# Optimization experiments

Hardware: AMD Instinct MI355X
Metric: run time of the kernel (lower is better)

## Reference

```python
import jax, jax.numpy as jnp
import numpy as np

D = 256   # input_dim (also per-head dim)
H = 8     # num_heads
B = 32
S = 1024


def setup_inputs() -> dict:
    key = jax.random.key(0)
    ks = jax.random.split(key, 9)
    scale = 1.0 / np.sqrt(D)
    x = jax.random.normal(ks[0], (B, S, D), dtype=jnp.float32)
    Wk = jax.random.normal(ks[1], (D, D * H), dtype=jnp.float32) * scale
    bk = jnp.zeros((D * H,), dtype=jnp.float32)
    Wv = jax.random.normal(ks[2], (D, D * H), dtype=jnp.float32) * scale
    bv = jnp.zeros((D * H,), dtype=jnp.float32)
    query = jax.random.normal(ks[3], (H, D), dtype=jnp.float32)
    Wo = jax.random.normal(ks[4], (D * H, D), dtype=jnp.float32) / np.sqrt(D * H)
    bo = jnp.zeros((D,), dtype=jnp.float32)
    return {"x": x, "Wk": Wk, "bk": bk, "Wv": Wv, "bv": bv,
            "query": query, "Wo": Wo, "bo": bo}


def reference(x, Wk, bk, Wv, bv, query, Wo, bo):
    b, s, _ = x.shape
    # keys/values: [B, S, H, D]
    keys = (x @ Wk + bk).reshape(b, s, H, D)
    values = (x @ Wv + bv).reshape(b, s, H, D)
    # per-head single-query scores over sequence: [B, S, H]
    scores = jnp.einsum("bshd,hd->bsh", keys, query)
    attn = jax.nn.softmax(scores, axis=1)
    # attention-pooled values per head: [B, H, D] -> concat [B, H*D]
    pooled = jnp.einsum("bsh,bshd->bhd", attn, values).reshape(b, H * D)
    return pooled @ Wo + bo
```

## Files before the change

### kernel.cpp

```cpp
#include <hip/hip_runtime.h>

#define D 256
#define H 8
#define B 32
#define S 1024
#define SCH 32
#define SCS 32
#define XPAD 4

#define OFF_QK   0
#define OFF_ML   2048
#define OFF_XWP  18432

__global__ void __launch_bounds__(256) k_prep(
        const float* __restrict__ Wk, const float* __restrict__ query,
        const float* __restrict__ bo, float* __restrict__ qk,
        float* __restrict__ out) {
    const int h  = blockIdx.x >> 5;
    const int kc = blockIdx.x & 31;
    const int t  = threadIdx.x;
    const int kl = t >> 5;
    const int dq = t & 31;
    const int k  = kc * 8 + kl;
    const int d0 = dq * 8;
    const float* wrow = Wk + (size_t)k * (D * H) + h * D + d0;
    const float* qrow = query + h * D + d0;
    const float4 w0 = *(const float4*)(wrow);
    const float4 w1 = *(const float4*)(wrow + 4);
    const float4 q0 = *(const float4*)(qrow);
    const float4 q1 = *(const float4*)(qrow + 4);
    float acc = w0.x * q0.x + w0.y * q0.y + w0.z * q0.z + w0.w * q0.w
              + w1.x * q1.x + w1.y * q1.y + w1.z * q1.z + w1.w * q1.w;
    #pragma unroll
    for (int msk = 1; msk < 32; msk <<= 1) acc += __shfl_xor(acc, msk);
    if (dq == 0) qk[h * D + k] = acc;
    if (h == 0) out[(size_t)kc * D + t] = bo[t];
}

__global__ void __launch_bounds__(256, 4) k_fused(
        const float* __restrict__ x, const float* __restrict__ qk,
        float* __restrict__ xwp, float2* __restrict__ mlbuf) {
    const int b  = blockIdx.x >> 5;
    const int c  = blockIdx.x & 31;
    const int s0 = c * SCS;
    const int t  = threadIdx.x;
    __shared__ float xL[SCS][D + XPAD];
    __shared__ float sc[SCS][H];
    {
        const int sl = t >> 3;
        const int dq = t & 7;
        const int d0 = dq * 32;
        const float* xrow = x + ((size_t)(b * S + s0 + sl)) * D + d0;
        float4 xr[8];
        #pragma unroll
        for (int j0 = 0; j0 < 8; j0++) {
            xr[j0] = *(const float4*)(xrow + j0 * 4);
            *(float4*)(&xL[sl][d0 + j0 * 4]) = xr[j0];
        }
        float accA[H];
        #pragma unroll
        for (int hh = 0; hh < H; hh++) {
            const float* qb = qk + hh * D + d0;
            float a = 0.f;
            #pragma unroll
            for (int j0 = 0; j0 < 8; j0++) {
                const float4 qv = *(const float4*)(qb + j0 * 4);
                a += xr[j0].x * qv.x + xr[j0].y * qv.y
                   + xr[j0].z * qv.z + xr[j0].w * qv.w;
            }
            accA[hh] = a;
        }
        #pragma unroll
        for (int hh = 0; hh < H; hh++) {
            accA[hh] += __shfl_xor(accA[hh], 1);
            accA[hh] += __shfl_xor(accA[hh], 2);
            accA[hh] += __shfl_xor(accA[hh], 4);
        }
        if (dq == 0) {
            #pragma unroll
            for (int hh = 0; hh < H; hh++) sc[sl][hh] = accA[hh];
        }
    }
    __syncthreads();

    {
        const int hh = t >> 5;
        const int u  = t & 31;
        const float v = sc[u][hh];
        float m = v;
        #pragma unroll
        for (int msk = 1; msk < 32; msk <<= 1) m = fmaxf(m, __shfl_xor(m, msk));
        const float e = __expf(v - m);
        float sum = e;
        #pragma unroll
        for (int msk = 1; msk < 32; msk <<= 1) sum += __shfl_xor(sum, msk);
        sc[u][hh] = e;
        if (u == 0) mlbuf[((size_t)(b * H + hh)) * SCH + c] = make_float2(m, sum);
    }
    __syncthreads();

    {
        float acc2[H] = {};
        #pragma unroll 8
        for (int s = 0; s < SCS; s++) {
            const float xv = xL[s][t];
            const float4 pa = *(const float4*)(&sc[s][0]);
            const float4 pb = *(const float4*)(&sc[s][4]);
            acc2[0] += pa.x * xv; acc2[1] += pa.y * xv;
            acc2[2] += pa.z * xv; acc2[3] += pa.w * xv;
            acc2[4] += pb.x * xv; acc2[5] += pb.y * xv;
            acc2[6] += pb.z * xv; acc2[7] += pb.w * xv;
        }
        #pragma unroll
        for (int hh = 0; hh < H; hh++)
            xwp[(((size_t)(b * H + hh)) * SCH + c) * D + t] = acc2[hh];
    }
}

__global__ void __launch_bounds__(256, 4) k_po(
        const float* __restrict__ xwp, const float2* __restrict__ mlbuf,
        const float* __restrict__ Wv, const float* __restrict__ bv,
        const float* __restrict__ Wo, float* __restrict__ out) {
    const int blk = blockIdx.x;
    const int dvq = blk & 3;
    const int bh  = blk >> 2;
    const int b = bh >> 3, h = bh & 7;
    const int t = threadIdx.x;
    __shared__ float scaleL[SCH];
    __shared__ float xwL[D];
    __shared__ float pp[256];
    __shared__ float pooledL[64];

    if (t < SCH) {
        const float2 ml = mlbuf[((size_t)(b * H + h)) * SCH + t];
        float M = ml.x;
        #pragma unroll
        for (int msk = 1; msk < 32; msk <<= 1) M = fmaxf(M, __shfl_xor(M, msk));
        const float p = __expf(ml.x - M);
        float L = ml.y * p;
        #pragma unroll
        for (int msk = 1; msk < 32; msk <<= 1) L += __shfl_xor(L, msk);
        scaleL[t] = p / L;
    }
    __syncthreads();
    {
        const float* xp = xwp + ((size_t)(b * H + h)) * SCH * D + t;
        float acc = 0.f;
        #pragma unroll 8
        for (int cc = 0; cc < SCH; cc++)
            acc += xp[(size_t)cc * D] * scaleL[cc];
        xwL[t] = acc;
    }
    __syncthreads();
    {
        const int kseg = t >> 6;
        const int dvl  = t & 63;
        const float* wp = Wv + (size_t)(kseg * 64) * (D * H) + h * D + dvq * 64 + dvl;
        float acc = 0.f;
        #pragma unroll 8
        for (int dd = 0; dd < 64; dd++)
            acc += xwL[kseg * 64 + dd] * wp[(size_t)dd * (D * H)];
        pp[t] = acc;
    }
    __syncthreads();
    if (t < 64)
        pooledL[t] = pp[t] + pp[t + 64] + pp[t + 128] + pp[t + 192]
                   + bv[h * D + dvq * 64 + t];
    __syncthreads();
    {
        const float* wo = Wo + (size_t)(h * D + dvq * 64) * D + t;
        float acc = 0.f;
        #pragma unroll 8
        for (int dv = 0; dv < 64; dv++)
            acc += pooledL[dv] * wo[(size_t)dv * D];
        atomicAdd(out + (size_t)b * D + t, acc);
    }
}

extern "C" void kernel_launch(void* const* d_in, const int* in_sizes, int n_in,
                              void* d_out, int out_size, void* d_ws, size_t ws_size,
                              hipStream_t stream) {
    const float* x     = (const float*)d_in[0];
    const float* Wk    = (const float*)d_in[1];
    const float* Wv    = (const float*)d_in[3];
    const float* bv    = (const float*)d_in[4];
    const float* query = (const float*)d_in[5];
    const float* Wo    = (const float*)d_in[6];
    const float* bo    = (const float*)d_in[7];
    float* out = (float*)d_out;
    float* ws  = (float*)d_ws;

    float*  qk    = ws + OFF_QK;
    float2* mlbuf = (float2*)(ws + OFF_ML);
    float*  xwp   = ws + OFF_XWP;

    k_prep<<<dim3(H * 32), dim3(256), 0, stream>>>(Wk, query, bo, qk, out);
    k_fused<<<dim3(B * SCH), dim3(256), 0, stream>>>(x, qk, xwp, mlbuf);
    k_po<<<dim3(B * H * 4), dim3(256), 0, stream>>>(xwp, mlbuf, Wv, bv, Wo, out);
}
```

Baseline: 129.6 us.

## Fuse three kernels into one persistent kernel with global atomic barriers

Merges the prep, fused-scoring and pooling/output kernels into a single 1024-block launch. Spin-wait counters in the workspace enforce the ordering: a global ready counter after the qk computation, and a per-batch done counter before the projection stage. The aim is to remove inter-kernel launch gaps and tail bubbles. In exchange it adds a memset launch and spin-waits whose correctness depends on all 1024 blocks being co-resident, with a spin cap as a fallback.

```diff
diff --git a/kernel.cpp b/kernel.cpp
--- a/kernel.cpp
+++ b/kernel.cpp
@@ -11,41 +11,63 @@
 #define OFF_QK   0
 #define OFF_ML   2048
 #define OFF_XWP  18432
-
-__global__ void __launch_bounds__(256) k_prep(
-        const float* __restrict__ Wk, const float* __restrict__ query,
-        const float* __restrict__ bo, float* __restrict__ qk,
-        float* __restrict__ out) {
-    const int h  = blockIdx.x >> 5;
-    const int kc = blockIdx.x & 31;
-    const int t  = threadIdx.x;
-    const int kl = t >> 5;
-    const int dq = t & 31;
-    const int k  = kc * 8 + kl;
-    const int d0 = dq * 8;
-    const float* wrow = Wk + (size_t)k * (D * H) + h * D + d0;
-    const float* qrow = query + h * D + d0;
-    const float4 w0 = *(const float4*)(wrow);
-    const float4 w1 = *(const float4*)(wrow + 4);
-    const float4 q0 = *(const float4*)(qrow);
-    const float4 q1 = *(const float4*)(qrow + 4);
-    float acc = w0.x * q0.x + w0.y * q0.y + w0.z * q0.z + w0.w * q0.w
-              + w1.x * q1.x + w1.y * q1.y + w1.z * q1.z + w1.w * q1.w;
-    #pragma unroll
-    for (int msk = 1; msk < 32; msk <<= 1) acc += __shfl_xor(acc, msk);
-    if (dq == 0) qk[h * D + k] = acc;
-    if (h == 0) out[(size_t)kc * D + t] = bo[t];
-}
-
-__global__ void __launch_bounds__(256, 4) k_fused(
-        const float* __restrict__ x, const float* __restrict__ qk,
-        float* __restrict__ xwp, float2* __restrict__ mlbuf) {
-    const int b  = blockIdx.x >> 5;
-    const int c  = blockIdx.x & 31;
-    const int s0 = c * SCS;
-    const int t  = threadIdx.x;
+#define OFF_CTR  2115584
+
+#define SPIN_CAP 4000000
+
+__global__ void __launch_bounds__(256, 4) k_all(
+        const float* __restrict__ x,  const float* __restrict__ Wk,
+        const float* __restrict__ query,
+        const float* __restrict__ Wv, const float* __restrict__ bv,
+        const float* __restrict__ Wo, const float* __restrict__ bo,
+        float* __restrict__ ws, float* __restrict__ out) {
     __shared__ float xL[SCS][D + XPAD];
     __shared__ float sc[SCS][H];
+
+    float*  qk    = ws + OFF_QK;
+    float2* mlbuf = (float2*)(ws + OFF_ML);
+    float*  xwp   = ws + OFF_XWP;
+    int*    ready = (int*)(ws + OFF_CTR);
+    int*    done  = ready + 1;
+
+    const int bid = blockIdx.x;
+    const int t   = threadIdx.x;
+    const int b   = bid >> 5;
+    const int c   = bid & 31;
+    const int s0  = c * SCS;
+
+    if (c == 0) out[(size_t)b * D + t] = bo[t];
+    if (bid < 256) {
+        const int h  = bid >> 5;
+        const int kc = bid & 31;
+        const int kl = t >> 5;
+        const int dq = t & 31;
+        const int k  = kc * 8 + kl;
+        const int d0 = dq * 8;
+        const float* wrow = Wk + (size_t)k * (D * H) + h * D + d0;
+        const float* qrow = query + h * D + d0;
+        const float4 w0 = *(const float4*)(wrow);
+        const float4 w1 = *(const float4*)(wrow + 4);
+        const float4 q0 = *(const float4*)(qrow);
+        const float4 q1 = *(const float4*)(qrow + 4);
+        float acc = w0.x * q0.x + w0.y * q0.y + w0.z * q0.z + w0.w * q0.w
+                  + w1.x * q1.x + w1.y * q1.y + w1.z * q1.z + w1.w * q1.w;
+        #pragma unroll
+        for (int msk = 1; msk < 32; msk <<= 1) acc += __shfl_xor(acc, msk);
+        if (dq == 0) qk[h * D + k] = acc;
+    }
+    __syncthreads();
+    if (t == 0) {
+        if (bid < 256)
+            __hip_atomic_fetch_add(ready, 1, __ATOMIC_ACQ_REL, __HIP_MEMORY_SCOPE_AGENT);
+        int it = 0;
+        while (__hip_atomic_load(ready, __ATOMIC_ACQUIRE, __HIP_MEMORY_SCOPE_AGENT) < 256) {
+            __builtin_amdgcn_s_sleep(1);
+            if (++it > SPIN_CAP) break;
+        }
+    }
+    __syncthreads();
+
     {
         const int sl = t >> 3;
         const int dq = t & 7;
@@ -82,7 +104,6 @@
         }
     }
     __syncthreads();
-
     {
         const int hh = t >> 5;
         const int u  = t & 31;
@@ -98,7 +119,6 @@
         if (u == 0) mlbuf[((size_t)(b * H + hh)) * SCH + c] = make_float2(m, sum);
     }
     __syncthreads();
-
     {
         float acc2[H] = {};
         #pragma unroll 8
@@ -115,65 +135,70 @@
         for (int hh = 0; hh < H; hh++)
             xwp[(((size_t)(b * H + hh)) * SCH + c) * D + t] = acc2[hh];
     }
-}
-
-__global__ void __launch_bounds__(256, 4) k_po(
-        const float* __restrict__ xwp, const float2* __restrict__ mlbuf,
-        const float* __restrict__ Wv, const float* __restrict__ bv,
-        const float* __restrict__ Wo, float* __restrict__ out) {
-    const int blk = blockIdx.x;
-    const int dvq = blk & 3;
-    const int bh  = blk >> 2;
-    const int b = bh >> 3, h = bh & 7;
-    const int t = threadIdx.x;
-    __shared__ float scaleL[SCH];
-    __shared__ float xwL[D];
-    __shared__ float pp[256];
-    __shared__ float pooledL[64];
-
-    if (t < SCH) {
-        const float2 ml = mlbuf[((size_t)(b * H + h)) * SCH + t];
-        float M = ml.x;
-        #pragma unroll
-        for (int msk = 1; msk < 32; msk <<= 1) M = fmaxf(M, __shfl_xor(M, msk));
-        const float p = __expf(ml.x - M);
-        float L = ml.y * p;
-        #pragma unroll
-        for (int msk = 1; msk < 32; msk <<= 1) L += __shfl_xor(L, msk);
-        scaleL[t] = p / L;
-    }
-    __syncthreads();
-    {
-        const float* xp = xwp + ((size_t)(b * H + h)) * SCH * D + t;
-        float acc = 0.f;
-        #pragma unroll 8
-        for (int cc = 0; cc < SCH; cc++)
-            acc += xp[(size_t)cc * D] * scaleL[cc];
-        xwL[t] = acc;
-    }
-    __syncthreads();
-    {
-        const int kseg = t >> 6;
-        const int dvl  = t & 63;
-        const float* wp = Wv + (size_t)(kseg * 64) * (D * H) + h * D + dvq * 64 + dvl;
-        float acc = 0.f;
-        #pragma unroll 8
-        for (int dd = 0; dd < 64; dd++)
-            acc += xwL[kseg * 64 + dd] * wp[(size_t)dd * (D * H)];
-        pp[t] = acc;
-    }
-    __syncthreads();
-    if (t < 64)
-        pooledL[t] = pp[t] + pp[t + 64] + pp[t + 128] + pp[t + 192]
-                   + bv[h * D + dvq * 64 + t];
-    __syncthreads();
-    {
-        const float* wo = Wo + (size_t)(h * D + dvq * 64) * D + t;
-        float acc = 0.f;
-        #pragma unroll 8
-        for (int dv = 0; dv < 64; dv++)
-            acc += pooledL[dv] * wo[(size_t)dv * D];
-        atomicAdd(out + (size_t)b * D + t, acc);
+
+    __syncthreads();
+    if (t == 0) {
+        __hip_atomic_fetch_add(done + b, 1, __ATOMIC_ACQ_REL, __HIP_MEMORY_SCOPE_AGENT);
+        int it = 0;
+        while (__hip_atomic_load(done + b, __ATOMIC_ACQUIRE, __HIP_MEMORY_SCOPE_AGENT) < 32) {
+            __builtin_amdgcn_s_sleep(1);
+            if (++it > SPIN_CAP) break;
+        }
+    }
+    __syncthreads();
+
+    {
+        const int h   = c >> 2;
+        const int dvq = c & 3;
+        float* scaleL  = &xL[0][0];
+        float* xwL     = scaleL + 32;
+        float* pp      = xwL + 256;
+        float* pooledL = pp + 256;
+
+        if (t < SCH) {
+            const float2 ml = mlbuf[((size_t)(b * H + h)) * SCH + t];
+            float M = ml.x;
+            #pragma unroll
+            for (int msk = 1; msk < 32; msk <<= 1) M = fmaxf(M, __shfl_xor(M, msk));
+            const float p = __expf(ml.x - M);
+            float L = ml.y * p;
+            #pragma unroll
+            for (int msk = 1; msk < 32; msk <<= 1) L += __shfl_xor(L, msk);
+            scaleL[t] = p / L;
+        }
+        __syncthreads();
+        {
+            const float* xp = xwp + ((size_t)(b * H + h)) * SCH * D + t;
+            float acc = 0.f;
+            #pragma unroll 8
+            for (int cc = 0; cc < SCH; cc++)
+                acc += xp[(size_t)cc * D] * scaleL[cc];
+            xwL[t] = acc;
+        }
+        __syncthreads();
+        {
+            const int kseg = t >> 6;
+            const int dvl  = t & 63;
+            const float* wp = Wv + (size_t)(kseg * 64) * (D * H) + h * D + dvq * 64 + dvl;
+            float acc = 0.f;
+            #pragma unroll 8
+            for (int dd = 0; dd < 64; dd++)
+                acc += xwL[kseg * 64 + dd] * wp[(size_t)dd * (D * H)];
+            pp[t] = acc;
+        }
+        __syncthreads();
+        if (t < 64)
+            pooledL[t] = pp[t] + pp[t + 64] + pp[t + 128] + pp[t + 192]
+                       + bv[h * D + dvq * 64 + t];
+        __syncthreads();
+        {
+            const float* wo = Wo + (size_t)(h * D + dvq * 64) * D + t;
+            float acc = 0.f;
+            #pragma unroll 8
+            for (int dv = 0; dv < 64; dv++)
+                acc += pooledL[dv] * wo[(size_t)dv * D];
+            atomicAdd(out + (size_t)b * D + t, acc);
+        }
     }
 }
 
@@ -190,11 +215,8 @@
     float* out = (float*)d_out;
     float* ws  = (float*)d_ws;
 
-    float*  qk    = ws + OFF_QK;
-    float2* mlbuf = (float2*)(ws + OFF_ML);
-    float*  xwp   = ws + OFF_XWP;
-
-    k_prep<<<dim3(H * 32), dim3(256), 0, stream>>>(Wk, query, bo, qk, out);
-    k_fused<<<dim3(B * SCH), dim3(256), 0, stream>>>(x, qk, xwp, mlbuf);
-    k_po<<<dim3(B * H * 4), dim3(256), 0, stream>>>(xwp, mlbuf, Wv, bv, Wo, out);
+    hipMemsetAsync((char*)d_ws + (size_t)OFF_CTR * sizeof(float), 0,
+                   (1 + B) * sizeof(int), stream);
+    k_all<<<dim3(B * SCH), dim3(256), 0, stream>>>(
+        x, Wk, query, Wv, bv, Wo, bo, ws, out);
 }
```

Measured after the change: 248.6 us. +91.9%, slower.

## Fuse pooling/output kernel into main kernel via per-batch spin barrier

Applied to the files above, without the earlier changes.

Merges the second and third kernels into one, with a per-batch atomic counter barrier: each block bumps its batch's counter and spins until all 32 chunks of that batch finish, then runs the Wv/Wo projection in place of the old kernel. The barrier counters are cleared with a memset before launch. The change also stages qk in shared memory, rotates the x load order per lane, and rereads x from global instead of keeping an x tile in LDS. It is meant to remove one launch and the gap between kernels, but it relies on all blocks of a batch being resident at once, and a spin cap bounds the wait, so a missed wait could give wrong results or stall.

```diff
diff --git a/kernel.cpp b/kernel.cpp
--- a/kernel.cpp
+++ b/kernel.cpp
@@ -6,11 +6,14 @@
 #define S 1024
 #define SCH 32
 #define SCS 32
-#define XPAD 4
 
 #define OFF_QK   0
 #define OFF_ML   2048
 #define OFF_XWP  18432
+#define OFF_DONE 2115584
+
+#define DONE_STRIDE 64
+#define SPIN_CAP 300000
 
 __global__ void __launch_bounds__(256) k_prep(
         const float* __restrict__ Wk, const float* __restrict__ query,
@@ -37,15 +40,26 @@
     if (h == 0) out[(size_t)kc * D + t] = bo[t];
 }
 
-__global__ void __launch_bounds__(256, 4) k_fused(
+__global__ void __launch_bounds__(256, 4) k_main(
         const float* __restrict__ x, const float* __restrict__ qk,
-        float* __restrict__ xwp, float2* __restrict__ mlbuf) {
-    const int b  = blockIdx.x >> 5;
-    const int c  = blockIdx.x & 31;
-    const int s0 = c * SCS;
-    const int t  = threadIdx.x;
-    __shared__ float xL[SCS][D + XPAD];
+        const float* __restrict__ Wv, const float* __restrict__ bv,
+        const float* __restrict__ Wo,
+        float* __restrict__ xwp, float2* __restrict__ mlbuf,
+        int* __restrict__ done, float* __restrict__ out) {
+    const int bid = blockIdx.x;
+    const int b   = bid >> 5;
+    const int c   = bid & 31;
+    const int s0  = c * SCS;
+    const int t   = threadIdx.x;
+    __shared__ float qkL[H * D];
     __shared__ float sc[SCS][H];
+    {
+        float4* q4 = (float4*)qkL;
+        q4[t]       = ((const float4*)qk)[t];
+        q4[t + 256] = ((const float4*)qk)[t + 256];
+    }
+    __syncthreads();
+
     {
         const int sl = t >> 3;
         const int dq = t & 7;
@@ -54,17 +68,18 @@
         float4 xr[8];
         #pragma unroll
         for (int j0 = 0; j0 < 8; j0++) {
-            xr[j0] = *(const float4*)(xrow + j0 * 4);
-            *(float4*)(&xL[sl][d0 + j0 * 4]) = xr[j0];
+            const int je = (j0 + dq) & 7;
+            xr[j0] = *(const float4*)(xrow + je * 4);
         }
         float accA[H];
         #pragma unroll
         for (int hh = 0; hh < H; hh++) {
-            const float* qb = qk + hh * D + d0;
+            const float* qb = &qkL[hh * D + d0];
             float a = 0.f;
             #pragma unroll
             for (int j0 = 0; j0 < 8; j0++) {
-                const float4 qv = *(const float4*)(qb + j0 * 4);
+                const int je = (j0 + dq) & 7;
+                const float4 qv = *(const float4*)(qb + je * 4);
                 a += xr[j0].x * qv.x + xr[j0].y * qv.y
                    + xr[j0].z * qv.z + xr[j0].w * qv.w;
             }
@@ -101,9 +116,10 @@
 
     {
         float acc2[H] = {};
+        const float* xp = x + ((size_t)(b * S + s0)) * D + t;
         #pragma unroll 8
         for (int s = 0; s < SCS; s++) {
-            const float xv = xL[s][t];
+            const float xv = xp[(size_t)s * D];
             const float4 pa = *(const float4*)(&sc[s][0]);
             const float4 pb = *(const float4*)(&sc[s][4]);
             acc2[0] += pa.x * xv; acc2[1] += pa.y * xv;
@@ -115,65 +131,71 @@
         for (int hh = 0; hh < H; hh++)
             xwp[(((size_t)(b * H + hh)) * SCH + c) * D + t] = acc2[hh];
     }
-}
-
-__global__ void __launch_bounds__(256, 4) k_po(
-        const float* __restrict__ xwp, const float2* __restrict__ mlbuf,
-        const float* __restrict__ Wv, const float* __restrict__ bv,
-        const float* __restrict__ Wo, float* __restrict__ out) {
-    const int blk = blockIdx.x;
-    const int dvq = blk & 3;
-    const int bh  = blk >> 2;
-    const int b = bh >> 3, h = bh & 7;
-    const int t = threadIdx.x;
-    __shared__ float scaleL[SCH];
-    __shared__ float xwL[D];
-    __shared__ float pp[256];
-    __shared__ float pooledL[64];
-
-    if (t < SCH) {
-        const float2 ml = mlbuf[((size_t)(b * H + h)) * SCH + t];
-        float M = ml.x;
-        #pragma unroll
-        for (int msk = 1; msk < 32; msk <<= 1) M = fmaxf(M, __shfl_xor(M, msk));
-        const float p = __expf(ml.x - M);
-        float L = ml.y * p;
-        #pragma unroll
-        for (int msk = 1; msk < 32; msk <<= 1) L += __shfl_xor(L, msk);
-        scaleL[t] = p / L;
-    }
-    __syncthreads();
-    {
-        const float* xp = xwp + ((size_t)(b * H + h)) * SCH * D + t;
-        float acc = 0.f;
-        #pragma unroll 8
-        for (int cc = 0; cc < SCH; cc++)
-            acc += xp[(size_t)cc * D] * scaleL[cc];
-        xwL[t] = acc;
-    }
-    __syncthreads();
-    {
-        const int kseg = t >> 6;
-        const int dvl  = t & 63;
-        const float* wp = Wv + (size_t)(kseg * 64) * (D * H) + h * D + dvq * 64 + dvl;
-        float acc = 0.f;
-        #pragma unroll 8
-        for (int dd = 0; dd < 64; dd++)
-            acc += xwL[kseg * 64 + dd] * wp[(size_t)dd * (D * H)];
-        pp[t] = acc;
-    }
-    __syncthreads();
-    if (t < 64)
-        pooledL[t] = pp[t] + pp[t + 64] + pp[t + 128] + pp[t + 192]
-                   + bv[h * D + dvq * 64 + t];
-    __syncthreads();
-    {
-        const float* wo = Wo + (size_t)(h * D + dvq * 64) * D + t;
-        float acc = 0.f;
-        #pragma unroll 8
-        for (int dv = 0; dv < 64; dv++)
-            acc += pooledL[dv] * wo[(size_t)dv * D];
-        atomicAdd(out + (size_t)b * D + t, acc);
+
+    __syncthreads();
+    if (t == 0) {
+        int* db = done + b * DONE_STRIDE;
+        __hip_atomic_fetch_add(db, 1, __ATOMIC_ACQ_REL, __HIP_MEMORY_SCOPE_AGENT);
+        int it = 0;
+        while (__hip_atomic_load(db, __ATOMIC_ACQUIRE, __HIP_MEMORY_SCOPE_AGENT) < 32) {
+            __builtin_amdgcn_s_sleep(32);
+            if (++it > SPIN_CAP) break;
+        }
+    }
+    __syncthreads();
+
+    {
+        const int h   = c >> 2;
+        const int dvq = c & 3;
+        float* scaleL  = qkL;
+        float* xwL     = qkL + 32;
+        float* pp      = qkL + 288;
+        float* pooledL = qkL + 544;
+
+        if (t < SCH) {
+            const float2 ml = mlbuf[((size_t)(b * H + h)) * SCH + t];
+            float M = ml.x;
+            #pragma unroll
+            for (int msk = 1; msk < 32; msk <<= 1) M = fmaxf(M, __shfl_xor(M, msk));
+            const float p = __expf(ml.x - M);
+            float L = ml.y * p;
+            #pragma unroll
+            for (int msk = 1; msk < 32; msk <<= 1) L += __shfl_xor(L, msk);
+            scaleL[t] = p / L;
+        }
+        __syncthreads();
+        {
+            const float* xp = xwp + ((size_t)(b * H + h)) * SCH * D + t;
+            float acc = 0.f;
+            #pragma unroll 8
+            for (int cc = 0; cc < SCH; cc++)
+                acc += xp[(size_t)cc * D] * scaleL[cc];
+            xwL[t] = acc;
+        }
+        __syncthreads();
+        {
+            const int kseg = t >> 6;
+            const int dvl  = t & 63;
+            const float* wp = Wv + (size_t)(kseg * 64) * (D * H) + h * D + dvq * 64 + dvl;
+            float acc = 0.f;
+            #pragma unroll 8
+            for (int dd = 0; dd < 64; dd++)
+                acc += xwL[kseg * 64 + dd] * wp[(size_t)dd * (D * H)];
+            pp[t] = acc;
+        }
+        __syncthreads();
+        if (t < 64)
+            pooledL[t] = pp[t] + pp[t + 64] + pp[t + 128] + pp[t + 192]
+                       + bv[h * D + dvq * 64 + t];
+        __syncthreads();
+        {
+            const float* wo = Wo + (size_t)(h * D + dvq * 64) * D + t;
+            float acc = 0.f;
+            #pragma unroll 8
+            for (int dv = 0; dv < 64; dv++)
+                acc += pooledL[dv] * wo[(size_t)dv * D];
+            atomicAdd(out + (size_t)b * D + t, acc);
+        }
     }
 }
 
@@ -193,8 +215,11 @@
     float*  qk    = ws + OFF_QK;
     float2* mlbuf = (float2*)(ws + OFF_ML);
     float*  xwp   = ws + OFF_XWP;
-
+    int*    done  = (int*)(ws + OFF_DONE);
+
+    hipMemsetAsync((char*)d_ws + (size_t)OFF_DONE * sizeof(float), 0,
+                   B * DONE_STRIDE * sizeof(int), stream);
     k_prep<<<dim3(H * 32), dim3(256), 0, stream>>>(Wk, query, bo, qk, out);
-    k_fused<<<dim3(B * SCH), dim3(256), 0, stream>>>(x, qk, xwp, mlbuf);
-    k_po<<<dim3(B * H * 4), dim3(256), 0, stream>>>(xwp, mlbuf, Wv, bv, Wo, out);
+    k_main<<<dim3(B * SCH), dim3(256), 0, stream>>>(
+        x, qk, Wv, bv, Wo, xwp, mlbuf, done, out);
 }
```

New measurement: 153.2 us. +18.2%, slower.

## Double sequence chunk size, stage qk in LDS, re-read x from global

Applied to the files above, without the earlier changes.

Sequence chunks per block grow from 32 to 64 rows, halving the chunk count and the partial-sum traffic that k_po must reduce. The projected query vectors (qk) are staged in shared memory once per block. The x tile is no longer cached in LDS; the pooling stage re-reads x from global memory and relies on L2 hits. This trades LDS footprint and occupancy limits for a second global read of x and fewer blocks.

```diff
diff --git a/kernel.cpp b/kernel.cpp
--- a/kernel.cpp
+++ b/kernel.cpp
@@ -4,13 +4,12 @@
 #define H 8
 #define B 32
 #define S 1024
-#define SCH 32
-#define SCS 32
-#define XPAD 4
+#define SCH 16
+#define SCS 64
 
 #define OFF_QK   0
 #define OFF_ML   2048
-#define OFF_XWP  18432
+#define OFF_XWP  10240
 
 __global__ void __launch_bounds__(256) k_prep(
         const float* __restrict__ Wk, const float* __restrict__ query,
@@ -37,48 +36,47 @@
     if (h == 0) out[(size_t)kc * D + t] = bo[t];
 }
 
-__global__ void __launch_bounds__(256, 4) k_fused(
+__global__ void __launch_bounds__(256) k_fused(
         const float* __restrict__ x, const float* __restrict__ qk,
         float* __restrict__ xwp, float2* __restrict__ mlbuf) {
-    const int b  = blockIdx.x >> 5;
-    const int c  = blockIdx.x & 31;
+    const int b  = blockIdx.x >> 4;
+    const int c  = blockIdx.x & 15;
     const int s0 = c * SCS;
     const int t  = threadIdx.x;
-    __shared__ float xL[SCS][D + XPAD];
+    __shared__ float qkL[H * D];
     __shared__ float sc[SCS][H];
     {
-        const int sl = t >> 3;
-        const int dq = t & 7;
-        const int d0 = dq * 32;
+        float4* q4 = (float4*)qkL;
+        q4[t]       = ((const float4*)qk)[t];
+        q4[t + 256] = ((const float4*)qk)[t + 256];
+    }
+    __syncthreads();
+
+    {
+        const int sl = t >> 2;
+        const int dq = t & 3;
+        const int d0 = dq * 64;
         const float* xrow = x + ((size_t)(b * S + s0 + sl)) * D + d0;
-        float4 xr[8];
-        #pragma unroll
-        for (int j0 = 0; j0 < 8; j0++) {
-            xr[j0] = *(const float4*)(xrow + j0 * 4);
-            *(float4*)(&xL[sl][d0 + j0 * 4]) = xr[j0];
-        }
-        float accA[H];
-        #pragma unroll
-        for (int hh = 0; hh < H; hh++) {
-            const float* qb = qk + hh * D + d0;
-            float a = 0.f;
+        float accA[H] = {};
+        #pragma unroll
+        for (int j0 = 0; j0 < 16; j0++) {
+            const int j = (j0 + dq * 4) & 15;
+            const float4 xv = *(const float4*)(xrow + j * 4);
             #pragma unroll
-            for (int j0 = 0; j0 < 8; j0++) {
-                const float4 qv = *(const float4*)(qb + j0 * 4);
-                a += xr[j0].x * qv.x + xr[j0].y * qv.y
-                   + xr[j0].z * qv.z + xr[j0].w * qv.w;
+            for (int hh = 0; hh < H; hh++) {
+                const float4 qv = *(const float4*)(&qkL[hh * D + d0 + j * 4]);
+                accA[hh] += xv.x * qv.x + xv.y * qv.y + xv.z * qv.z + xv.w * qv.w;
             }
-            accA[hh] = a;
         }
         #pragma unroll
         for (int hh = 0; hh < H; hh++) {
             accA[hh] += __shfl_xor(accA[hh], 1);
             accA[hh] += __shfl_xor(accA[hh], 2);
-            accA[hh] += __shfl_xor(accA[hh], 4);
         }
         if (dq == 0) {
             #pragma unroll
-            for (int hh = 0; hh < H; hh++) sc[sl][hh] = accA[hh];
+            for (int hh = 0; hh < H; hh++)
+                sc[sl][hh] = accA[hh];
         }
     }
     __syncthreads();
@@ -86,24 +84,26 @@
     {
         const int hh = t >> 5;
         const int u  = t & 31;
-        const float v = sc[u][hh];
-        float m = v;
+        const float v0 = sc[u][hh], v1 = sc[u + 32][hh];
+        float m = fmaxf(v0, v1);
         #pragma unroll
         for (int msk = 1; msk < 32; msk <<= 1) m = fmaxf(m, __shfl_xor(m, msk));
-        const float e = __expf(v - m);
-        float sum = e;
+        const float e0 = __expf(v0 - m), e1 = __expf(v1 - m);
+        float sum = e0 + e1;
         #pragma unroll
         for (int msk = 1; msk < 32; msk <<= 1) sum += __shfl_xor(sum, msk);
-        sc[u][hh] = e;
+        sc[u][hh] = e0;
+        sc[u + 32][hh] = e1;
         if (u == 0) mlbuf[((size_t)(b * H + hh)) * SCH + c] = make_float2(m, sum);
     }
     __syncthreads();
 
     {
         float acc2[H] = {};
-        #pragma unroll 8
+        const float* xp = x + ((size_t)(b * S + s0)) * D + t;
+        #pragma unroll 4
         for (int s = 0; s < SCS; s++) {
-            const float xv = xL[s][t];
+            const float xv = xp[(size_t)s * D];
             const float4 pa = *(const float4*)(&sc[s][0]);
             const float4 pb = *(const float4*)(&sc[s][4]);
             acc2[0] += pa.x * xv; acc2[1] += pa.y * xv;
@@ -135,18 +135,18 @@
         const float2 ml = mlbuf[((size_t)(b * H + h)) * SCH + t];
         float M = ml.x;
         #pragma unroll
-        for (int msk = 1; msk < 32; msk <<= 1) M = fmaxf(M, __shfl_xor(M, msk));
+        for (int msk = 1; msk < 16; msk <<= 1) M = fmaxf(M, __shfl_xor(M, msk));
         const float p = __expf(ml.x - M);
         float L = ml.y * p;
         #pragma unroll
-        for (int msk = 1; msk < 32; msk <<= 1) L += __shfl_xor(L, msk);
+        for (int msk = 1; msk < 16; msk <<= 1) L += __shfl_xor(L, msk);
         scaleL[t] = p / L;
     }
     __syncthreads();
     {
         const float* xp = xwp + ((size_t)(b * H + h)) * SCH * D + t;
         float acc = 0.f;
-        #pragma unroll 8
+        #pragma unroll
         for (int cc = 0; cc < SCH; cc++)
             acc += xp[(size_t)cc * D] * scaleL[cc];
         xwL[t] = acc;
```

Result: faster. 110.3 us (-14.8%).
